# Performance work log

Measured on AMD Instinct MI355X. Metric: run time of the kernel, lower is better.

Reference implementation:

```python
import jax, jax.numpy as jnp
import numpy as np
import math

EPS = 1e-5  # torch nn.LayerNorm default
MODEL_DIM = 1024


def _layernorm(x, g, b):
    mu = jnp.mean(x, axis=-1, keepdims=True)
    var = jnp.mean(jnp.square(x - mu), axis=-1, keepdims=True)
    return (x - mu) * jax.lax.rsqrt(var + EPS) * g + b


def _block(x, g, b, w, bias):
    # LayerNorm -> Linear -> exact (erf) GELU, matching torch nn.GELU default
    h = _layernorm(x, g, b)
    h = h @ w.T + bias
    return jax.nn.gelu(h, approximate=False)


def setup_inputs() -> dict:
    key = jax.random.key(0)
    ks = jax.random.split(key, 4)
    N, F = 262144, 6
    dims = [F, 128, 512, 1024]
    inp = {"x": jax.random.normal(ks[0], (N, F), dtype=jnp.float32)}
    for i in range(3):
        fan_in, fan_out = dims[i], dims[i + 1]
        bound = 1.0 / math.sqrt(fan_in)
        inp[f"ln{i}_g"] = jnp.ones((fan_in,), dtype=jnp.float32)
        inp[f"ln{i}_b"] = jnp.zeros((fan_in,), dtype=jnp.float32)
        inp[f"w{i}"] = jax.random.uniform(ks[i + 1], (fan_out, fan_in), dtype=jnp.float32, minval=-bound, maxval=bound)
        inp[f"b{i}"] = jnp.zeros((fan_out,), dtype=jnp.float32)
    return inp


def reference(x, ln0_g, ln0_b, w0, b0, ln1_g, ln1_b, w1, b1, ln2_g, ln2_b, w2, b2):
    h = _block(x, ln0_g, ln0_b, w0, b0)
    h = _block(h, ln1_g, ln1_b, w1, b1)
    h = _block(h, ln2_g, ln2_b, w2, b2)
    return h * jnp.float32(math.sqrt(MODEL_DIM))
```

## Files before the change

### kernel.cpp

```cpp
#include <hip/hip_runtime.h>

typedef __attribute__((ext_vector_type(8))) __bf16 bf16x8;
typedef __attribute__((ext_vector_type(4))) float f32x4;
typedef __attribute__((ext_vector_type(8))) unsigned short ushort8;
typedef __attribute__((ext_vector_type(4))) float floatx4;

__device__ __forceinline__ unsigned short f2bf(float f) {
    return __builtin_bit_cast(unsigned short, (__bf16)f);
}
__device__ __forceinline__ float bf2f(unsigned short s) {
    return (float)__builtin_bit_cast(__bf16, s);
}
__device__ __forceinline__ float gelu_f(float v) {
    return 0.5f * v * (1.0f + erff(v * 0.70710678118654752440f));
}

__device__ __forceinline__ char* lds_at(unsigned short* base, int rowBytes, int row, int col) {
    return (char*)base + row * rowBytes + ((col * 2) ^ ((row & 7) << 4));
}

template<bool BF>
__device__ __forceinline__ bf16x8 load_w8(const void* wp, int off) {
    if constexpr (BF) {
        return *(const bf16x8*)((const unsigned short*)wp + off);
    } else {
        const float* p = (const float*)wp + off;
        floatx4 lo = *(const floatx4*)p;
        floatx4 hi = *(const floatx4*)(p + 4);
        union { unsigned short u[8]; bf16x8 v; } pk;
        #pragma unroll
        for (int e = 0; e < 4; ++e) { pk.u[e] = f2bf(lo[e]); pk.u[4 + e] = f2bf(hi[e]); }
        return pk.v;
    }
}

__device__ __forceinline__ void load_afrag(bf16x8 (&dst)[4], unsigned short* lds,
                                           int rowBytes, int lr, int k0) {
    #pragma unroll
    for (int i = 0; i < 4; ++i)
        dst[i] = *(const bf16x8*)lds_at(lds, rowBytes, i * 16 + lr, k0);
}
template<bool BF>
__device__ __forceinline__ void load_bfrag(bf16x8 (&dst)[4], const void* wp,
                                           int ldk, int ncol, int k0) {
    #pragma unroll
    for (int j = 0; j < 4; ++j)
        dst[j] = load_w8<BF>(wp, (ncol + j * 16) * ldk + k0);
}
__device__ __forceinline__ void mm16(f32x4 (&acc)[4][4], const bf16x8 (&a)[4], const bf16x8 (&b)[4]) {
    #pragma unroll
    for (int i = 0; i < 4; ++i)
        #pragma unroll
        for (int j = 0; j < 4; ++j)
            acc[i][j] = __builtin_amdgcn_mfma_f32_16x16x32_bf16(a[i], b[j], acc[i][j], 0, 0, 0);
}

__global__ void prep_kernel(const float* __restrict__ w1, const float* __restrict__ w2,
                            unsigned short* __restrict__ w1b, unsigned short* __restrict__ w2b) {
    int i = blockIdx.x * 256 + threadIdx.x;
    if (i < 512 * 128) w1b[i] = f2bf(w1[i]);
    int j = i - 512 * 128;
    if (j >= 0 && j < 1024 * 512) w2b[j] = f2bf(w2[j]);
}

template<bool BF>
__global__ __launch_bounds__(256, 2) void fused_mlp(
    const float* __restrict__ x,
    const float* __restrict__ ln0g, const float* __restrict__ ln0b,
    const float* __restrict__ w0,   const float* __restrict__ b0,
    const float* __restrict__ ln1g, const float* __restrict__ ln1b,
    const void*  __restrict__ w1p,  const float* __restrict__ b1,
    const float* __restrict__ ln2g, const float* __restrict__ ln2b,
    const void*  __restrict__ w2p,  const float* __restrict__ b2,
    float* __restrict__ out)
{
    __shared__ alignas(16) unsigned short h1n[64 * 128];
    __shared__ alignas(16) unsigned short h2s[64 * 512];

    const int tid  = threadIdx.x;
    const int lane = tid & 63;
    const int wv   = tid >> 6;
    const long rowbase = (long)blockIdx.x * 64;

    {
        const int r = tid >> 2;
        const int q = tid & 3;
        const long grow = rowbase + r;
        float xv[6], xn[6];
        #pragma unroll
        for (int f = 0; f < 6; ++f) xv[f] = x[grow * 6 + f];
        float mu = 0.f;
        #pragma unroll
        for (int f = 0; f < 6; ++f) mu += xv[f];
        mu *= (1.0f / 6.0f);
        float var = 0.f;
        #pragma unroll
        for (int f = 0; f < 6; ++f) { float d = xv[f] - mu; var += d * d; }
        var *= (1.0f / 6.0f);
        const float rstd = rsqrtf(var + 1e-5f);
        #pragma unroll
        for (int f = 0; f < 6; ++f) xn[f] = (xv[f] - mu) * rstd * ln0g[f] + ln0b[f];

        float h0[32];
        float s1 = 0.f, s2 = 0.f;
        #pragma unroll
        for (int o = 0; o < 32; ++o) {
            const int n = q * 32 + o;
            float a = b0[n];
            #pragma unroll
            for (int f = 0; f < 6; ++f) a += xn[f] * w0[n * 6 + f];
            a = gelu_f(a);
            h0[o] = a; s1 += a; s2 += a * a;
        }
        float* scr = (float*)h2s;
        scr[tid] = s1; scr[256 + tid] = s2;
        __syncthreads();
        const int b4 = tid & ~3;
        s1 = scr[b4] + scr[b4 + 1] + scr[b4 + 2] + scr[b4 + 3];
        s2 = scr[256 + b4] + scr[256 + b4 + 1] + scr[256 + b4 + 2] + scr[256 + b4 + 3];
        const float mu1   = s1 * (1.0f / 128.0f);
        const float var1  = s2 * (1.0f / 128.0f) - mu1 * mu1;
        const float rstd1 = rsqrtf(var1 + 1e-5f);
        #pragma unroll
        for (int o8 = 0; o8 < 4; ++o8) {
            union { unsigned short u[8]; ushort8 v; } pk;
            #pragma unroll
            for (int e = 0; e < 8; ++e) {
                const int n = q * 32 + o8 * 8 + e;
                pk.u[e] = f2bf((h0[o8 * 8 + e] - mu1) * rstd1 * ln1g[n] + ln1b[n]);
            }
            *(ushort8*)lds_at(h1n, 256, r, q * 32 + o8 * 8) = pk.v;
        }
    }
    __syncthreads();

    {
        const int lr = lane & 15;
        const int lk = (lane >> 4) * 8;
        const int mr = (lane >> 4) * 4;
        #pragma unroll 1
        for (int c = 0; c < 2; ++c) {
            const int n0 = wv * 128 + c * 64;
            f32x4 acc[4][4] = {};
            bf16x8 aP[4], bP[4], aQ[4], bQ[4];
            load_afrag(aP, h1n, 256, lr, lk);
            load_bfrag<BF>(bP, w1p, 128, n0 + lr, lk);
            load_afrag(aQ, h1n, 256, lr, 32 + lk);
            load_bfrag<BF>(bQ, w1p, 128, n0 + lr, 32 + lk);
            mm16(acc, aP, bP);
            load_afrag(aP, h1n, 256, lr, 64 + lk);
            load_bfrag<BF>(bP, w1p, 128, n0 + lr, 64 + lk);
            mm16(acc, aQ, bQ);
            load_afrag(aQ, h1n, 256, lr, 96 + lk);
            load_bfrag<BF>(bQ, w1p, 128, n0 + lr, 96 + lk);
            mm16(acc, aP, bP);
            mm16(acc, aQ, bQ);
            #pragma unroll
            for (int j = 0; j < 4; ++j) {
                const int n = n0 + j * 16 + lr;
                const float bias = b1[n];
                #pragma unroll
                for (int i = 0; i < 4; ++i)
                    #pragma unroll
                    for (int rr = 0; rr < 4; ++rr) {
                        const int m = i * 16 + mr + rr;
                        *(unsigned short*)lds_at(h2s, 1024, m, n) = f2bf(gelu_f(acc[i][j][rr] + bias));
                    }
            }
        }
    }
    __syncthreads();

    {
        const int r = tid >> 2;
        const int q = tid & 3;
        float s1 = 0.f, s2 = 0.f;
        #pragma unroll
        for (int g = 0; g < 16; ++g) {
            ushort8 v = *(const ushort8*)lds_at(h2s, 1024, r, q * 128 + g * 8);
            #pragma unroll
            for (int e = 0; e < 8; ++e) { const float f = bf2f(v[e]); s1 += f; s2 += f * f; }
        }
        float* scr = (float*)h1n;
        scr[tid] = s1; scr[256 + tid] = s2;
        __syncthreads();
        const int b4 = tid & ~3;
        s1 = scr[b4] + scr[b4 + 1] + scr[b4 + 2] + scr[b4 + 3];
        s2 = scr[256 + b4] + scr[256 + b4 + 1] + scr[256 + b4 + 2] + scr[256 + b4 + 3];
        const float mu   = s1 * (1.0f / 512.0f);
        const float var  = s2 * (1.0f / 512.0f) - mu * mu;
        const float rstd = rsqrtf(var + 1e-5f);
        #pragma unroll
        for (int g = 0; g < 16; ++g) {
            const int col0 = q * 128 + g * 8;
            char* p = lds_at(h2s, 1024, r, col0);
            ushort8 v = *(const ushort8*)p;
            union { unsigned short u[8]; ushort8 vv; } pk;
            #pragma unroll
            for (int e = 0; e < 8; ++e)
                pk.u[e] = f2bf((bf2f(v[e]) - mu) * rstd * ln2g[col0 + e] + ln2b[col0 + e]);
            *(ushort8*)p = pk.vv;
        }
    }
    __syncthreads();

    {
        const int lr = lane & 15;
        const int lk = (lane >> 4) * 8;
        const int mr = (lane >> 4) * 4;
        #pragma unroll 1
        for (int c = 0; c < 4; ++c) {
            const int n0 = wv * 256 + c * 64;
            f32x4 acc[4][4] = {};
            bf16x8 aP[4], bP[4], aQ[4], bQ[4];
            load_afrag(aP, h2s, 1024, lr, lk);
            load_bfrag<BF>(bP, w2p, 512, n0 + lr, lk);
            #pragma unroll
            for (int ks = 0; ks < 16; ks += 2) {
                const int k0 = ks * 32 + lk;
                load_afrag(aQ, h2s, 1024, lr, k0 + 32);
                load_bfrag<BF>(bQ, w2p, 512, n0 + lr, k0 + 32);
                mm16(acc, aP, bP);
                if (ks + 2 < 16) {
                    load_afrag(aP, h2s, 1024, lr, k0 + 64);
                    load_bfrag<BF>(bP, w2p, 512, n0 + lr, k0 + 64);
                }
                mm16(acc, aQ, bQ);
            }
            #pragma unroll
            for (int j = 0; j < 4; ++j) {
                const int n = n0 + j * 16 + lr;
                const float bias = b2[n];
                #pragma unroll
                for (int i = 0; i < 4; ++i)
                    #pragma unroll
                    for (int rr = 0; rr < 4; ++rr) {
                        const int m = i * 16 + mr + rr;
                        const float v = gelu_f(acc[i][j][rr] + bias) * 32.0f;
                        __builtin_nontemporal_store(v, &out[(rowbase + m) * 1024 + n]);
                    }
            }
        }
    }
}

extern "C" void kernel_launch(void* const* d_in, const int* in_sizes, int n_in,
                              void* d_out, int out_size, void* d_ws, size_t ws_size,
                              hipStream_t stream)
{
    const float* x    = (const float*)d_in[0];
    const float* ln0g = (const float*)d_in[1];
    const float* ln0b = (const float*)d_in[2];
    const float* w0   = (const float*)d_in[3];
    const float* b0   = (const float*)d_in[4];
    const float* ln1g = (const float*)d_in[5];
    const float* ln1b = (const float*)d_in[6];
    const float* w1   = (const float*)d_in[7];
    const float* b1   = (const float*)d_in[8];
    const float* ln2g = (const float*)d_in[9];
    const float* ln2b = (const float*)d_in[10];
    const float* w2   = (const float*)d_in[11];
    const float* b2   = (const float*)d_in[12];
    float* out = (float*)d_out;

    const int rows = in_sizes[0] / 6;
    const int grid = rows / 64;
    const size_t need = (size_t)(512 * 128 + 1024 * 512) * sizeof(unsigned short);

    if (ws_size >= need) {
        unsigned short* w1b = (unsigned short*)d_ws;
        unsigned short* w2b = w1b + 512 * 128;
        prep_kernel<<<dim3((512 * 128 + 1024 * 512 + 255) / 256), dim3(256), 0, stream>>>(w1, w2, w1b, w2b);
        fused_mlp<true><<<dim3(grid), dim3(256), 0, stream>>>(
            x, ln0g, ln0b, w0, b0, ln1g, ln1b, (const void*)w1b, b1,
            ln2g, ln2b, (const void*)w2b, b2, out);
    } else {
        fused_mlp<false><<<dim3(grid), dim3(256), 0, stream>>>(
            x, ln0g, ln0b, w0, b0, ln1g, ln1b, (const void*)w1, b1,
            ln2g, ln2b, (const void*)w2, b2, out);
    }
}
```

Before: 1.390 ms.

## Use one thread per row for LayerNorm stages and approximate final GELU

Layer-0 compute and the layer-2 LayerNorm now run on only the first 64 threads, one row each, with rolled loops. This removes the intra-block scratch reductions and the extra barriers. Layer-0 outputs are computed twice (once for the statistics, once for the normalized write), which trades extra work for lower register pressure. The final layer's exact erf GELU is replaced by a sigmoid-based exp2/rcp approximation, and the nontemporal output stores become plain stores. The approximation changes the numerics on the output, and leaving 3 of 4 waves idle during those stages cuts parallelism.

After: 1.472 ms. 6.0% more time.

```diff
diff --git a/kernel.cpp b/kernel.cpp
--- a/kernel.cpp
+++ b/kernel.cpp
@@ -13,6 +13,11 @@
 }
 __device__ __forceinline__ float gelu_f(float v) {
     return 0.5f * v * (1.0f + erff(v * 0.70710678118654752440f));
+}
+__device__ __forceinline__ float gelu_fast(float v) {
+    const float z = v * (2.3022077f + 0.1029432f * v * v);
+    const float u = __builtin_amdgcn_exp2f(-z);
+    return v * __builtin_amdgcn_rcpf(1.0f + u);
 }
 
 __device__ __forceinline__ char* lds_at(unsigned short* base, int rowBytes, int row, int col) {
@@ -82,9 +87,8 @@
     const int wv   = tid >> 6;
     const long rowbase = (long)blockIdx.x * 64;
 
-    {
-        const int r = tid >> 2;
-        const int q = tid & 3;
+    if (tid < 64) {
+        const int r = tid;
         const long grow = rowbase + r;
         float xv[6], xn[6];
         #pragma unroll
@@ -101,35 +105,32 @@
         #pragma unroll
         for (int f = 0; f < 6; ++f) xn[f] = (xv[f] - mu) * rstd * ln0g[f] + ln0b[f];
 
-        float h0[32];
         float s1 = 0.f, s2 = 0.f;
-        #pragma unroll
-        for (int o = 0; o < 32; ++o) {
-            const int n = q * 32 + o;
+        #pragma unroll 1
+        for (int n = 0; n < 128; ++n) {
             float a = b0[n];
             #pragma unroll
             for (int f = 0; f < 6; ++f) a += xn[f] * w0[n * 6 + f];
             a = gelu_f(a);
-            h0[o] = a; s1 += a; s2 += a * a;
-        }
-        float* scr = (float*)h2s;
-        scr[tid] = s1; scr[256 + tid] = s2;
-        __syncthreads();
-        const int b4 = tid & ~3;
-        s1 = scr[b4] + scr[b4 + 1] + scr[b4 + 2] + scr[b4 + 3];
-        s2 = scr[256 + b4] + scr[256 + b4 + 1] + scr[256 + b4 + 2] + scr[256 + b4 + 3];
+            s1 += a; s2 += a * a;
+        }
         const float mu1   = s1 * (1.0f / 128.0f);
         const float var1  = s2 * (1.0f / 128.0f) - mu1 * mu1;
         const float rstd1 = rsqrtf(var1 + 1e-5f);
-        #pragma unroll
-        for (int o8 = 0; o8 < 4; ++o8) {
+
+        #pragma unroll 1
+        for (int g = 0; g < 16; ++g) {
             union { unsigned short u[8]; ushort8 v; } pk;
             #pragma unroll
             for (int e = 0; e < 8; ++e) {
-                const int n = q * 32 + o8 * 8 + e;
-                pk.u[e] = f2bf((h0[o8 * 8 + e] - mu1) * rstd1 * ln1g[n] + ln1b[n]);
-            }
-            *(ushort8*)lds_at(h1n, 256, r, q * 32 + o8 * 8) = pk.v;
+                const int n = g * 8 + e;
+                float a = b0[n];
+                #pragma unroll
+                for (int f = 0; f < 6; ++f) a += xn[f] * w0[n * 6 + f];
+                a = gelu_f(a);
+                pk.u[e] = f2bf((a - mu1) * rstd1 * ln1g[n] + ln1b[n]);
+            }
+            *(ushort8*)lds_at(h1n, 256, r, g * 8) = pk.v;
         }
     }
     __syncthreads();
@@ -171,34 +172,28 @@
     }
     __syncthreads();
 
-    {
-        const int r = tid >> 2;
-        const int q = tid & 3;
+    if (tid < 64) {
+        const int r = tid;
         float s1 = 0.f, s2 = 0.f;
-        #pragma unroll
-        for (int g = 0; g < 16; ++g) {
-            ushort8 v = *(const ushort8*)lds_at(h2s, 1024, r, q * 128 + g * 8);
+        #pragma unroll 1
+        for (int g = 0; g < 64; ++g) {
+            ushort8 v = *(const ushort8*)lds_at(h2s, 1024, r, g * 8);
             #pragma unroll
             for (int e = 0; e < 8; ++e) { const float f = bf2f(v[e]); s1 += f; s2 += f * f; }
         }
-        float* scr = (float*)h1n;
-        scr[tid] = s1; scr[256 + tid] = s2;
-        __syncthreads();
-        const int b4 = tid & ~3;
-        s1 = scr[b4] + scr[b4 + 1] + scr[b4 + 2] + scr[b4 + 3];
-        s2 = scr[256 + b4] + scr[256 + b4 + 1] + scr[256 + b4 + 2] + scr[256 + b4 + 3];
         const float mu   = s1 * (1.0f / 512.0f);
         const float var  = s2 * (1.0f / 512.0f) - mu * mu;
         const float rstd = rsqrtf(var + 1e-5f);
-        #pragma unroll
-        for (int g = 0; g < 16; ++g) {
-            const int col0 = q * 128 + g * 8;
-            char* p = lds_at(h2s, 1024, r, col0);
+        #pragma unroll 1
+        for (int g = 0; g < 64; ++g) {
+            char* p = lds_at(h2s, 1024, r, g * 8);
             ushort8 v = *(const ushort8*)p;
             union { unsigned short u[8]; ushort8 vv; } pk;
             #pragma unroll
-            for (int e = 0; e < 8; ++e)
-                pk.u[e] = f2bf((bf2f(v[e]) - mu) * rstd * ln2g[col0 + e] + ln2b[col0 + e]);
+            for (int e = 0; e < 8; ++e) {
+                const int n = g * 8 + e;
+                pk.u[e] = f2bf((bf2f(v[e]) - mu) * rstd * ln2g[n] + ln2b[n]);
+            }
             *(ushort8*)p = pk.vv;
         }
     }
@@ -236,8 +231,7 @@
                     #pragma unroll
                     for (int rr = 0; rr < 4; ++rr) {
                         const int m = i * 16 + mr + rr;
-                        const float v = gelu_f(acc[i][j][rr] + bias) * 32.0f;
-                        __builtin_nontemporal_store(v, &out[(rowbase + m) * 1024 + n]);
+                        out[(rowbase + m) * 1024 + n] = gelu_fast(acc[i][j][rr] + bias) * 32.0f;
                     }
             }
         }
```
